# Performance work log

Measured on AMD Instinct MI355X. Metric: run time of the kernel, lower is better.

## Reference

```python
import jax, jax.numpy as jnp
import numpy as np

INPUT_DIM = 256
OUTPUT_DIM = 256
DEGREE = 7


def setup_inputs() -> dict:
    key = jax.random.key(0)
    k1, k2 = jax.random.split(key)
    x = jax.random.normal(k1, (16, 2048, INPUT_DIM), dtype=jnp.float32)
    std = 1.0 / (INPUT_DIM * (DEGREE + 1))
    hermite_coeffs = std * jax.random.normal(k2, (INPUT_DIM, OUTPUT_DIM, DEGREE + 1), dtype=jnp.float32)
    return {"x": x, "hermite_coeffs": hermite_coeffs}


def reference(x, hermite_coeffs):
    a, b, c = x.shape
    degree = hermite_coeffs.shape[2] - 1
    xf = jnp.tanh(x.reshape(-1, c))  # [N, input_dim]
    hs = [jnp.ones_like(xf)]
    if degree > 0:
        hs.append(2.0 * xf)
    for i in range(2, degree + 1):
        hs.append(2.0 * xf * hs[-1] - 2.0 * (i - 1) * hs[-2])
    hermite = jnp.stack(hs, axis=-1)  # [N, input_dim, degree+1]
    y = jnp.einsum('bid,iod->bo', hermite, hermite_coeffs)
    return y.reshape(a, b, hermite_coeffs.shape[1])
```

## Files before the change

kernel.cpp:

```cpp
#include <hip/hip_runtime.h>
#include <hip/hip_bf16.h>
#include <math.h>

#define INPUT_DIM 256
#define OUT_DIM   256
#define NDEG      8
#define KTOT      (INPUT_DIM * NDEG)
#define NROWS     (16 * 2048)

#define BM  128
#define BK  64
#define NK  (KTOT / BK)
#define SUPER 4
#define NSUP  (NK / SUPER)
#define CHUNK_ELEMS 16384

typedef __bf16 bf16x8 __attribute__((ext_vector_type(8)));
typedef float  f32x16 __attribute__((ext_vector_type(16)));

__global__ __launch_bounds__(256) void reorder_coeffs(const float* __restrict__ C,
                                                      __bf16* __restrict__ Bt) {
    int g = blockIdx.x * 256 + threadIdx.x;
    int i = g >> 8;
    int o = g & 255;
    const float4* src = (const float4*)(C + (size_t)i * (OUT_DIM * NDEG) + o * NDEG);
    float4 a = src[0];
    float4 b = src[1];
    bf16x8 v;
    v[0] = (__bf16)a.x; v[1] = (__bf16)a.y; v[2] = (__bf16)a.z; v[3] = (__bf16)a.w;
    v[4] = (__bf16)b.x; v[5] = (__bf16)b.y; v[6] = (__bf16)b.z; v[7] = (__bf16)b.w;
    int kc = i >> 3;
    int p  = i & 7;
    int s  = p >> 1;
    int hh = p & 1;
    int cc = o >> 6;
    int ni = (o >> 5) & 1;
    int l31 = o & 31;
    size_t dst = (size_t)kc * CHUNK_ELEMS + (s * 4 + cc) * 1024 + ni * 512 + hh * 256 + l31 * 8;
    *(bf16x8*)(Bt + dst) = v;
}

__device__ __forceinline__ bf16x8 featurize(float xs) {
    float e = __expf(2.0f * xs);
    float t = 1.0f - 2.0f / (e + 1.0f);
    bf16x8 v;
    float hm2 = 1.0f;
    float hm1 = 2.0f * t;
    v[0] = (__bf16)hm2;
    v[1] = (__bf16)hm1;
    #pragma unroll
    for (int d = 2; d < 8; ++d) {
        float h = 2.0f * t * hm1 - 2.0f * (float)(d - 1) * hm2;
        v[d] = (__bf16)h;
        hm2 = hm1; hm1 = h;
    }
    return v;
}

#define BARRIER() do {                                             \
    asm volatile("s_waitcnt lgkmcnt(0)" ::: "memory");             \
    __builtin_amdgcn_s_barrier();                                  \
    asm volatile("" ::: "memory");                                 \
} while (0)

__global__ __launch_bounds__(512, 2) void hermite_mfma(const float* __restrict__ x,
                                                       const __bf16* __restrict__ Bt,
                                                       float* __restrict__ out) {
    __shared__ __align__(16) __bf16 Alds[2][SUPER * 8192];

    const int tid  = threadIdx.x;
    const int bm   = blockIdx.x;
    const int wave = tid >> 6;
    const int mr   = wave >> 2;
    const int c    = wave & 3;
    const int lane = tid & 63;
    const int l31  = lane & 31;
    const int h    = lane >> 5;

    const int m  = tid & 127;
    const int pg = tid >> 7;
    const float* xptr = x + (size_t)(bm * BM + m) * INPUT_DIM + pg * 8;

    const __bf16* bbase = Bt + (size_t)c * 1024 + lane * 8;

    f32x16 acc[2][2] = {};
    bf16x8 bfr0[4][2];
    bf16x8 bfr1[4][2];

#define BLOAD(DST, KC)                                                       \
    if ((KC) < NK) {                                                         \
        const __bf16* g = bbase + (size_t)(KC) * CHUNK_ELEMS;                \
        _Pragma("unroll")                                                    \
        for (int s = 0; s < 4; ++s) {                                        \
            DST[s][0] = *(const bf16x8*)(g + s * 4096);                      \
            DST[s][1] = *(const bf16x8*)(g + s * 4096 + 512);                \
        }                                                                    \
    }

#define FEATW(NB, J, XS)                                                     \
    *(bf16x8*)(&Alds[NB][pg * 8192 + (J) * 1024 + m * 8]) = featurize(XS)

#define CHUNK_COMPUTE(CB, CC, CUR)                                           \
    _Pragma("unroll")                                                        \
    for (int s4 = 0; s4 < 4; ++s4) {                                         \
        bf16x8 af0 = *(const bf16x8*)(&Alds[CB][(CC) * 8192 + (2 * s4 + h) * 1024 + mr * 512 + l31 * 8]);       \
        bf16x8 af1 = *(const bf16x8*)(&Alds[CB][(CC) * 8192 + (2 * s4 + h) * 1024 + mr * 512 + 256 + l31 * 8]); \
        acc[0][0] = __builtin_amdgcn_mfma_f32_32x32x16_bf16(af0, CUR[s4][0], acc[0][0], 0, 0, 0); \
        acc[0][1] = __builtin_amdgcn_mfma_f32_32x32x16_bf16(af0, CUR[s4][1], acc[0][1], 0, 0, 0); \
        acc[1][0] = __builtin_amdgcn_mfma_f32_32x32x16_bf16(af1, CUR[s4][0], acc[1][0], 0, 0, 0); \
        acc[1][1] = __builtin_amdgcn_mfma_f32_32x32x16_bf16(af1, CUR[s4][1], acc[1][1], 0, 0, 0); \
    }

    float4 xq0 = *(const float4*)(xptr);
    float4 xq1 = *(const float4*)(xptr + 4);
    BLOAD(bfr0, 0);
    float4 xa0 = *(const float4*)(xptr + 32);
    float4 xa1 = *(const float4*)(xptr + 36);
    float4 xb0 = xa0, xb1 = xa1;
    FEATW(0, 0, xq0.x); FEATW(0, 1, xq0.y); FEATW(0, 2, xq0.z); FEATW(0, 3, xq0.w);
    FEATW(0, 4, xq1.x); FEATW(0, 5, xq1.y); FEATW(0, 6, xq1.z); FEATW(0, 7, xq1.w);
    BARRIER();

#define SUPER_STEP(S, CB, NB, XC0, XC1, XN0, XN1)                            \
    {                                                                        \
        const bool dofeat = (S) + 1 < NSUP;                                  \
        BLOAD(bfr1, (S) * 4 + 1);                                            \
        if (dofeat) { FEATW(NB, 0, XC0.x); FEATW(NB, 1, XC0.y); }            \
        CHUNK_COMPUTE(CB, 0, bfr0);                                          \
        BLOAD(bfr0, (S) * 4 + 2);                                            \
        if (dofeat) { FEATW(NB, 2, XC0.z); FEATW(NB, 3, XC0.w); }            \
        CHUNK_COMPUTE(CB, 1, bfr1);                                          \
        BLOAD(bfr1, (S) * 4 + 3);                                            \
        if (dofeat) { FEATW(NB, 4, XC1.x); FEATW(NB, 5, XC1.y); }            \
        CHUNK_COMPUTE(CB, 2, bfr0);                                          \
        BLOAD(bfr0, (S) * 4 + 4);                                            \
        if (dofeat) { FEATW(NB, 6, XC1.z); FEATW(NB, 7, XC1.w); }            \
        if ((S) + 2 < NSUP) {                                                \
            XN0 = *(const float4*)(xptr + ((S) + 2) * 32);                   \
            XN1 = *(const float4*)(xptr + ((S) + 2) * 32 + 4);               \
        }                                                                    \
        CHUNK_COMPUTE(CB, 3, bfr1);                                          \
        BARRIER();                                                           \
    }

    for (int sp = 0; sp < NSUP; sp += 2) {
        SUPER_STEP(sp,     0, 1, xa0, xa1, xb0, xb1);
        SUPER_STEP(sp + 1, 1, 0, xb0, xb1, xa0, xa1);
    }
#undef SUPER_STEP
#undef CHUNK_COMPUTE
#undef FEATW
#undef BLOAD

    #pragma unroll
    for (int mi = 0; mi < 2; ++mi)
        #pragma unroll
        for (int ni = 0; ni < 2; ++ni) {
            #pragma unroll
            for (int r = 0; r < 16; ++r) {
                int rl  = (r & 3) + 8 * (r >> 2) + 4 * h;
                int row = bm * BM + mr * 64 + mi * 32 + rl;
                out[(size_t)row * OUT_DIM + c * 64 + ni * 32 + l31] = acc[mi][ni][r];
            }
        }
}

extern "C" void kernel_launch(void* const* d_in, const int* in_sizes, int n_in,
                              void* d_out, int out_size, void* d_ws, size_t ws_size,
                              hipStream_t stream) {
    const float* x = (const float*)d_in[0];
    const float* C = (const float*)d_in[1];
    float* out = (float*)d_out;
    __bf16* Bt = (__bf16*)d_ws;

    reorder_coeffs<<<dim3((INPUT_DIM * OUT_DIM) / 256), dim3(256), 0, stream>>>(C, Bt);
    hermite_mfma<<<dim3(NROWS / BM), dim3(512), 0, stream>>>(x, Bt, out);
}
```

Measured before the change: 115.1 us.

## Halve row tile to 64 and raise occupancy to four blocks per CU

Cuts the M tile from 128 to 64 rows, so each wave computes one 32-row MFMA strip instead of two and each thread featurizes 4 inputs per super-step instead of 8. The LDS footprint halves and launch bounds ask for 4 blocks per CU, doubling the grid to 512 blocks. The goal is more waves and blocks in flight to hide latency and balance work across CUs. The cost is that each B fragment loaded from global memory feeds half as many MFMAs, which doubles total coefficient traffic.

```diff
diff --git a/kernel.cpp b/kernel.cpp
--- a/kernel.cpp
+++ b/kernel.cpp
@@ -8,12 +8,14 @@
 #define KTOT      (INPUT_DIM * NDEG)
 #define NROWS     (16 * 2048)
 
-#define BM  128
+#define BM  64
 #define BK  64
 #define NK  (KTOT / BK)
 #define SUPER 4
 #define NSUP  (NK / SUPER)
 #define CHUNK_ELEMS 16384
+#define APAGE 512
+#define ACHUNK (8 * APAGE)
 
 typedef __bf16 bf16x8 __attribute__((ext_vector_type(8)));
 typedef float  f32x16 __attribute__((ext_vector_type(16)));
@@ -35,7 +37,8 @@
     int hh = p & 1;
     int cc = o >> 6;
     int ni = (o >> 5) & 1;
-    int l31 = o & 31;
+    int l31 = o & 255 & 31;
+    l31 = o & 31;
     size_t dst = (size_t)kc * CHUNK_ELEMS + (s * 4 + cc) * 1024 + ni * 512 + hh * 256 + l31 * 8;
     *(bf16x8*)(Bt + dst) = v;
 }
@@ -63,10 +66,10 @@
     asm volatile("" ::: "memory");                                 \
 } while (0)
 
-__global__ __launch_bounds__(512, 2) void hermite_mfma(const float* __restrict__ x,
+__global__ __launch_bounds__(512, 4) void hermite_mfma(const float* __restrict__ x,
                                                        const __bf16* __restrict__ Bt,
                                                        float* __restrict__ out) {
-    __shared__ __align__(16) __bf16 Alds[2][SUPER * 8192];
+    __shared__ __align__(16) __bf16 Alds[2][SUPER * ACHUNK];
 
     const int tid  = threadIdx.x;
     const int bm   = blockIdx.x;
@@ -77,13 +80,13 @@
     const int l31  = lane & 31;
     const int h    = lane >> 5;
 
-    const int m  = tid & 127;
-    const int pg = tid >> 7;
-    const float* xptr = x + (size_t)(bm * BM + m) * INPUT_DIM + pg * 8;
+    const int m  = tid & 63;
+    const int pg = tid >> 6;
+    const float* xptr = x + (size_t)(bm * BM + m) * INPUT_DIM + pg * 4;
 
     const __bf16* bbase = Bt + (size_t)c * 1024 + lane * 8;
 
-    f32x16 acc[2][2] = {};
+    f32x16 acc[2] = {};
     bf16x8 bfr0[4][2];
     bf16x8 bfr1[4][2];
 
@@ -98,54 +101,47 @@
     }
 
 #define FEATW(NB, J, XS)                                                     \
-    *(bf16x8*)(&Alds[NB][pg * 8192 + (J) * 1024 + m * 8]) = featurize(XS)
+    *(bf16x8*)(&Alds[NB][(pg * 4 + (J)) * APAGE + m * 8]) = featurize(XS)
 
 #define CHUNK_COMPUTE(CB, CC, CUR)                                           \
     _Pragma("unroll")                                                        \
     for (int s4 = 0; s4 < 4; ++s4) {                                         \
-        bf16x8 af0 = *(const bf16x8*)(&Alds[CB][(CC) * 8192 + (2 * s4 + h) * 1024 + mr * 512 + l31 * 8]);       \
-        bf16x8 af1 = *(const bf16x8*)(&Alds[CB][(CC) * 8192 + (2 * s4 + h) * 1024 + mr * 512 + 256 + l31 * 8]); \
-        acc[0][0] = __builtin_amdgcn_mfma_f32_32x32x16_bf16(af0, CUR[s4][0], acc[0][0], 0, 0, 0); \
-        acc[0][1] = __builtin_amdgcn_mfma_f32_32x32x16_bf16(af0, CUR[s4][1], acc[0][1], 0, 0, 0); \
-        acc[1][0] = __builtin_amdgcn_mfma_f32_32x32x16_bf16(af1, CUR[s4][0], acc[1][0], 0, 0, 0); \
-        acc[1][1] = __builtin_amdgcn_mfma_f32_32x32x16_bf16(af1, CUR[s4][1], acc[1][1], 0, 0, 0); \
+        bf16x8 af = *(const bf16x8*)(&Alds[CB][((CC) * 8 + 2 * s4 + h) * APAGE + mr * 256 + l31 * 8]); \
+        acc[0] = __builtin_amdgcn_mfma_f32_32x32x16_bf16(af, CUR[s4][0], acc[0], 0, 0, 0); \
+        acc[1] = __builtin_amdgcn_mfma_f32_32x32x16_bf16(af, CUR[s4][1], acc[1], 0, 0, 0); \
     }
 
-    float4 xq0 = *(const float4*)(xptr);
-    float4 xq1 = *(const float4*)(xptr + 4);
+    float4 xq = *(const float4*)(xptr);
     BLOAD(bfr0, 0);
-    float4 xa0 = *(const float4*)(xptr + 32);
-    float4 xa1 = *(const float4*)(xptr + 36);
-    float4 xb0 = xa0, xb1 = xa1;
-    FEATW(0, 0, xq0.x); FEATW(0, 1, xq0.y); FEATW(0, 2, xq0.z); FEATW(0, 3, xq0.w);
-    FEATW(0, 4, xq1.x); FEATW(0, 5, xq1.y); FEATW(0, 6, xq1.z); FEATW(0, 7, xq1.w);
+    float4 xa = *(const float4*)(xptr + 32);
+    float4 xb = xa;
+    FEATW(0, 0, xq.x); FEATW(0, 1, xq.y); FEATW(0, 2, xq.z); FEATW(0, 3, xq.w);
     BARRIER();
 
-#define SUPER_STEP(S, CB, NB, XC0, XC1, XN0, XN1)                            \
+#define SUPER_STEP(S, CB, NB, XC, XN)                                        \
     {                                                                        \
         const bool dofeat = (S) + 1 < NSUP;                                  \
         BLOAD(bfr1, (S) * 4 + 1);                                            \
-        if (dofeat) { FEATW(NB, 0, XC0.x); FEATW(NB, 1, XC0.y); }            \
+        if (dofeat) { FEATW(NB, 0, XC.x); }                                  \
         CHUNK_COMPUTE(CB, 0, bfr0);                                          \
         BLOAD(bfr0, (S) * 4 + 2);                                            \
-        if (dofeat) { FEATW(NB, 2, XC0.z); FEATW(NB, 3, XC0.w); }            \
+        if (dofeat) { FEATW(NB, 1, XC.y); }                                  \
         CHUNK_COMPUTE(CB, 1, bfr1);                                          \
         BLOAD(bfr1, (S) * 4 + 3);                                            \
-        if (dofeat) { FEATW(NB, 4, XC1.x); FEATW(NB, 5, XC1.y); }            \
+        if (dofeat) { FEATW(NB, 2, XC.z); }                                  \
         CHUNK_COMPUTE(CB, 2, bfr0);                                          \
         BLOAD(bfr0, (S) * 4 + 4);                                            \
-        if (dofeat) { FEATW(NB, 6, XC1.z); FEATW(NB, 7, XC1.w); }            \
+        if (dofeat) { FEATW(NB, 3, XC.w); }                                  \
         if ((S) + 2 < NSUP) {                                                \
-            XN0 = *(const float4*)(xptr + ((S) + 2) * 32);                   \
-            XN1 = *(const float4*)(xptr + ((S) + 2) * 32 + 4);               \
+            XN = *(const float4*)(xptr + ((S) + 2) * 32);                    \
         }                                                                    \
         CHUNK_COMPUTE(CB, 3, bfr1);                                          \
         BARRIER();                                                           \
     }
 
     for (int sp = 0; sp < NSUP; sp += 2) {
-        SUPER_STEP(sp,     0, 1, xa0, xa1, xb0, xb1);
-        SUPER_STEP(sp + 1, 1, 0, xb0, xb1, xa0, xa1);
+        SUPER_STEP(sp,     0, 1, xa, xb);
+        SUPER_STEP(sp + 1, 1, 0, xb, xa);
     }
 #undef SUPER_STEP
 #undef CHUNK_COMPUTE
@@ -153,16 +149,14 @@
 #undef BLOAD
 
     #pragma unroll
-    for (int mi = 0; mi < 2; ++mi)
+    for (int ni = 0; ni < 2; ++ni) {
         #pragma unroll
-        for (int ni = 0; ni < 2; ++ni) {
-            #pragma unroll
-            for (int r = 0; r < 16; ++r) {
-                int rl  = (r & 3) + 8 * (r >> 2) + 4 * h;
-                int row = bm * BM + mr * 64 + mi * 32 + rl;
-                out[(size_t)row * OUT_DIM + c * 64 + ni * 32 + l31] = acc[mi][ni][r];
-            }
+        for (int r = 0; r < 16; ++r) {
+            int rl  = (r & 3) + 8 * (r >> 2) + 4 * h;
+            int row = bm * BM + mr * 32 + rl;
+            out[(size_t)row * OUT_DIM + c * 64 + ni * 32 + l31] = acc[ni][r];
         }
+    }
 }
 
 extern "C" void kernel_launch(void* const* d_in, const int* in_sizes, int n_in,
```

New measurement: 136.1 us. +18.2%, slower.

## Stagger featurization across even/odd waves and raise priority around MFMA blocks

Applied to the files above, without the earlier changes.

Even waves now featurize the next LDS buffer at the start of each super-step and odd waves do it after the second chunk, so the two wave groups sharing a SIMD alternate between VALU/transcendental work and MFMA work. Each MFMA chunk is also wrapped in s_setprio(1)/s_setprio(0) so waves issuing matrix ops are favoured by the scheduler. The intent is better overlap of the Hermite feature computation with matrix-core execution. The cost is two code paths, which grows code size and may raise register pressure, and the priority changes could delay the loads that feed later chunks.

```diff
diff --git a/kernel.cpp b/kernel.cpp
--- a/kernel.cpp
+++ b/kernel.cpp
@@ -101,14 +101,18 @@
     *(bf16x8*)(&Alds[NB][pg * 8192 + (J) * 1024 + m * 8]) = featurize(XS)
 
 #define CHUNK_COMPUTE(CB, CC, CUR)                                           \
-    _Pragma("unroll")                                                        \
-    for (int s4 = 0; s4 < 4; ++s4) {                                         \
-        bf16x8 af0 = *(const bf16x8*)(&Alds[CB][(CC) * 8192 + (2 * s4 + h) * 1024 + mr * 512 + l31 * 8]);       \
-        bf16x8 af1 = *(const bf16x8*)(&Alds[CB][(CC) * 8192 + (2 * s4 + h) * 1024 + mr * 512 + 256 + l31 * 8]); \
-        acc[0][0] = __builtin_amdgcn_mfma_f32_32x32x16_bf16(af0, CUR[s4][0], acc[0][0], 0, 0, 0); \
-        acc[0][1] = __builtin_amdgcn_mfma_f32_32x32x16_bf16(af0, CUR[s4][1], acc[0][1], 0, 0, 0); \
-        acc[1][0] = __builtin_amdgcn_mfma_f32_32x32x16_bf16(af1, CUR[s4][0], acc[1][0], 0, 0, 0); \
-        acc[1][1] = __builtin_amdgcn_mfma_f32_32x32x16_bf16(af1, CUR[s4][1], acc[1][1], 0, 0, 0); \
+    {                                                                        \
+        __builtin_amdgcn_s_setprio(1);                                       \
+        _Pragma("unroll")                                                    \
+        for (int s4 = 0; s4 < 4; ++s4) {                                     \
+            bf16x8 af0 = *(const bf16x8*)(&Alds[CB][(CC) * 8192 + (2 * s4 + h) * 1024 + mr * 512 + l31 * 8]);       \
+            bf16x8 af1 = *(const bf16x8*)(&Alds[CB][(CC) * 8192 + (2 * s4 + h) * 1024 + mr * 512 + 256 + l31 * 8]); \
+            acc[0][0] = __builtin_amdgcn_mfma_f32_32x32x16_bf16(af0, CUR[s4][0], acc[0][0], 0, 0, 0); \
+            acc[0][1] = __builtin_amdgcn_mfma_f32_32x32x16_bf16(af0, CUR[s4][1], acc[0][1], 0, 0, 0); \
+            acc[1][0] = __builtin_amdgcn_mfma_f32_32x32x16_bf16(af1, CUR[s4][0], acc[1][0], 0, 0, 0); \
+            acc[1][1] = __builtin_amdgcn_mfma_f32_32x32x16_bf16(af1, CUR[s4][1], acc[1][1], 0, 0, 0); \
+        }                                                                    \
+        __builtin_amdgcn_s_setprio(0);                                       \
     }
 
     float4 xq0 = *(const float4*)(xptr);
@@ -121,33 +125,63 @@
     FEATW(0, 4, xq1.x); FEATW(0, 5, xq1.y); FEATW(0, 6, xq1.z); FEATW(0, 7, xq1.w);
     BARRIER();
 
-#define SUPER_STEP(S, CB, NB, XC0, XC1, XN0, XN1)                            \
+#define SUPER_STEP_E(S, CB, NB, XC0, XC1, XN0, XN1)                          \
+    {                                                                        \
+        const bool dofeat = (S) + 1 < NSUP;                                  \
+        if (dofeat) { FEATW(NB, 0, XC0.x); FEATW(NB, 1, XC0.y);              \
+                      FEATW(NB, 2, XC0.z); FEATW(NB, 3, XC0.w); }            \
+        BLOAD(bfr1, (S) * 4 + 1);                                            \
+        if (dofeat) { FEATW(NB, 4, XC1.x); FEATW(NB, 5, XC1.y);              \
+                      FEATW(NB, 6, XC1.z); FEATW(NB, 7, XC1.w); }            \
+        CHUNK_COMPUTE(CB, 0, bfr0);                                          \
+        BLOAD(bfr0, (S) * 4 + 2);                                            \
+        CHUNK_COMPUTE(CB, 1, bfr1);                                          \
+        BLOAD(bfr1, (S) * 4 + 3);                                            \
+        CHUNK_COMPUTE(CB, 2, bfr0);                                          \
+        BLOAD(bfr0, (S) * 4 + 4);                                            \
+        if ((S) + 2 < NSUP) {                                                \
+            XN0 = *(const float4*)(xptr + ((S) + 2) * 32);                   \
+            XN1 = *(const float4*)(xptr + ((S) + 2) * 32 + 4);               \
+        }                                                                    \
+        CHUNK_COMPUTE(CB, 3, bfr1);                                          \
+        BARRIER();                                                           \
+    }
+
+#define SUPER_STEP_O(S, CB, NB, XC0, XC1, XN0, XN1)                          \
     {                                                                        \
         const bool dofeat = (S) + 1 < NSUP;                                  \
         BLOAD(bfr1, (S) * 4 + 1);                                            \
-        if (dofeat) { FEATW(NB, 0, XC0.x); FEATW(NB, 1, XC0.y); }            \
         CHUNK_COMPUTE(CB, 0, bfr0);                                          \
         BLOAD(bfr0, (S) * 4 + 2);                                            \
-        if (dofeat) { FEATW(NB, 2, XC0.z); FEATW(NB, 3, XC0.w); }            \
         CHUNK_COMPUTE(CB, 1, bfr1);                                          \
+        if (dofeat) { FEATW(NB, 0, XC0.x); FEATW(NB, 1, XC0.y);              \
+                      FEATW(NB, 2, XC0.z); FEATW(NB, 3, XC0.w);              \
+                      FEATW(NB, 4, XC1.x); FEATW(NB, 5, XC1.y);              \
+                      FEATW(NB, 6, XC1.z); FEATW(NB, 7, XC1.w); }            \
         BLOAD(bfr1, (S) * 4 + 3);                                            \
-        if (dofeat) { FEATW(NB, 4, XC1.x); FEATW(NB, 5, XC1.y); }            \
         CHUNK_COMPUTE(CB, 2, bfr0);                                          \
-        BLOAD(bfr0, (S) * 4 + 4);                                            \
-        if (dofeat) { FEATW(NB, 6, XC1.z); FEATW(NB, 7, XC1.w); }            \
         if ((S) + 2 < NSUP) {                                                \
             XN0 = *(const float4*)(xptr + ((S) + 2) * 32);                   \
             XN1 = *(const float4*)(xptr + ((S) + 2) * 32 + 4);               \
         }                                                                    \
+        BLOAD(bfr0, (S) * 4 + 4);                                            \
         CHUNK_COMPUTE(CB, 3, bfr1);                                          \
         BARRIER();                                                           \
     }
 
-    for (int sp = 0; sp < NSUP; sp += 2) {
-        SUPER_STEP(sp,     0, 1, xa0, xa1, xb0, xb1);
-        SUPER_STEP(sp + 1, 1, 0, xb0, xb1, xa0, xa1);
-    }
-#undef SUPER_STEP
+    if ((wave & 1) == 0) {
+        for (int sp = 0; sp < NSUP; sp += 2) {
+            SUPER_STEP_E(sp,     0, 1, xa0, xa1, xb0, xb1);
+            SUPER_STEP_E(sp + 1, 1, 0, xb0, xb1, xa0, xa1);
+        }
+    } else {
+        for (int sp = 0; sp < NSUP; sp += 2) {
+            SUPER_STEP_O(sp,     0, 1, xa0, xa1, xb0, xb1);
+            SUPER_STEP_O(sp + 1, 1, 0, xb0, xb1, xa0, xa1);
+        }
+    }
+#undef SUPER_STEP_E
+#undef SUPER_STEP_O
 #undef CHUNK_COMPUTE
 #undef FEATW
 #undef BLOAD
```

After: 117.0 us. About the same (+1.7%).

## Restructure K-loop into barrier-separated phases with batched LDS reads and MFMA priority

Applied to the files above, without the earlier changes.

Each chunk becomes a phase: all eight A fragments are read from LDS up front, then featurization writes and the next B global load are issued, then a workgroup barrier, then 16 MFMAs run at raised wave priority (s_setprio), then another waitcnt plus barrier. sched_barrier fences keep the compiler from interleaving memory and MFMA sections. The aim is to have waves alternate between memory and math phases so that MFMA issue is less often stalled by interleaved LDS and global traffic. The cost is two barriers per chunk instead of one per superstep, which adds synchronization overhead and more live registers.

```diff
diff --git a/kernel.cpp b/kernel.cpp
--- a/kernel.cpp
+++ b/kernel.cpp
@@ -57,12 +57,6 @@
     return v;
 }
 
-#define BARRIER() do {                                             \
-    asm volatile("s_waitcnt lgkmcnt(0)" ::: "memory");             \
-    __builtin_amdgcn_s_barrier();                                  \
-    asm volatile("" ::: "memory");                                 \
-} while (0)
-
 __global__ __launch_bounds__(512, 2) void hermite_mfma(const float* __restrict__ x,
                                                        const __bf16* __restrict__ Bt,
                                                        float* __restrict__ out) {
@@ -100,15 +94,52 @@
 #define FEATW(NB, J, XS)                                                     \
     *(bf16x8*)(&Alds[NB][pg * 8192 + (J) * 1024 + m * 8]) = featurize(XS)
 
-#define CHUNK_COMPUTE(CB, CC, CUR)                                           \
-    _Pragma("unroll")                                                        \
-    for (int s4 = 0; s4 < 4; ++s4) {                                         \
-        bf16x8 af0 = *(const bf16x8*)(&Alds[CB][(CC) * 8192 + (2 * s4 + h) * 1024 + mr * 512 + l31 * 8]);       \
-        bf16x8 af1 = *(const bf16x8*)(&Alds[CB][(CC) * 8192 + (2 * s4 + h) * 1024 + mr * 512 + 256 + l31 * 8]); \
-        acc[0][0] = __builtin_amdgcn_mfma_f32_32x32x16_bf16(af0, CUR[s4][0], acc[0][0], 0, 0, 0); \
-        acc[0][1] = __builtin_amdgcn_mfma_f32_32x32x16_bf16(af0, CUR[s4][1], acc[0][1], 0, 0, 0); \
-        acc[1][0] = __builtin_amdgcn_mfma_f32_32x32x16_bf16(af1, CUR[s4][0], acc[1][0], 0, 0, 0); \
-        acc[1][1] = __builtin_amdgcn_mfma_f32_32x32x16_bf16(af1, CUR[s4][1], acc[1][1], 0, 0, 0); \
+#define MFMA_S(AF0, AF1, CURS)                                               \
+    acc[0][0] = __builtin_amdgcn_mfma_f32_32x32x16_bf16(AF0, CURS[0], acc[0][0], 0, 0, 0); \
+    acc[0][1] = __builtin_amdgcn_mfma_f32_32x32x16_bf16(AF0, CURS[1], acc[0][1], 0, 0, 0); \
+    acc[1][0] = __builtin_amdgcn_mfma_f32_32x32x16_bf16(AF1, CURS[0], acc[1][0], 0, 0, 0); \
+    acc[1][1] = __builtin_amdgcn_mfma_f32_32x32x16_bf16(AF1, CURS[1], acc[1][1], 0, 0, 0);
+
+#define PHASE(S, CB, NB, CC, CUR, NXT, DOF, FJ, XS0, XS1, XPRE)              \
+    {                                                                        \
+        const __bf16* ab = &Alds[CB][(CC) * 8192 + mr * 512 + l31 * 8];      \
+        bf16x8 a0 = *(const bf16x8*)(ab + (0 + h) * 1024);                   \
+        bf16x8 a1 = *(const bf16x8*)(ab + (0 + h) * 1024 + 256);             \
+        bf16x8 a2 = *(const bf16x8*)(ab + (2 + h) * 1024);                   \
+        bf16x8 a3 = *(const bf16x8*)(ab + (2 + h) * 1024 + 256);             \
+        bf16x8 a4 = *(const bf16x8*)(ab + (4 + h) * 1024);                   \
+        bf16x8 a5 = *(const bf16x8*)(ab + (4 + h) * 1024 + 256);             \
+        bf16x8 a6 = *(const bf16x8*)(ab + (6 + h) * 1024);                   \
+        bf16x8 a7 = *(const bf16x8*)(ab + (6 + h) * 1024 + 256);             \
+        if (DOF) { FEATW(NB, (FJ), XS0); FEATW(NB, (FJ) + 1, XS1); }         \
+        BLOAD(NXT, (S) * 4 + (CC) + 1);                                      \
+        XPRE                                                                 \
+        __builtin_amdgcn_sched_barrier(0);                                   \
+        __builtin_amdgcn_s_barrier();                                        \
+        __builtin_amdgcn_sched_barrier(0);                                   \
+        __builtin_amdgcn_s_setprio(1);                                       \
+        MFMA_S(a0, a1, CUR[0])                                               \
+        MFMA_S(a2, a3, CUR[1])                                               \
+        MFMA_S(a4, a5, CUR[2])                                               \
+        MFMA_S(a6, a7, CUR[3])                                               \
+        __builtin_amdgcn_s_setprio(0);                                       \
+        __builtin_amdgcn_sched_barrier(0);                                   \
+        asm volatile("s_waitcnt lgkmcnt(0)" ::: "memory");                   \
+        __builtin_amdgcn_s_barrier();                                        \
+        asm volatile("" ::: "memory");                                       \
+    }
+
+#define SUPER_STEP(S, CB, NB, XC0, XC1, XN0, XN1)                            \
+    {                                                                        \
+        const bool dofeat = (S) + 1 < NSUP;                                  \
+        PHASE(S, CB, NB, 0, bfr0, bfr1, dofeat, 0, XC0.x, XC0.y, )           \
+        PHASE(S, CB, NB, 1, bfr1, bfr0, dofeat, 2, XC0.z, XC0.w, )           \
+        PHASE(S, CB, NB, 2, bfr0, bfr1, dofeat, 4, XC1.x, XC1.y, )           \
+        PHASE(S, CB, NB, 3, bfr1, bfr0, dofeat, 6, XC1.z, XC1.w,             \
+              if ((S) + 2 < NSUP) {                                          \
+                  XN0 = *(const float4*)(xptr + ((S) + 2) * 32);             \
+                  XN1 = *(const float4*)(xptr + ((S) + 2) * 32 + 4);         \
+              })                                                             \
     }
 
     float4 xq0 = *(const float4*)(xptr);
@@ -119,36 +150,17 @@
     float4 xb0 = xa0, xb1 = xa1;
     FEATW(0, 0, xq0.x); FEATW(0, 1, xq0.y); FEATW(0, 2, xq0.z); FEATW(0, 3, xq0.w);
     FEATW(0, 4, xq1.x); FEATW(0, 5, xq1.y); FEATW(0, 6, xq1.z); FEATW(0, 7, xq1.w);
-    BARRIER();
-
-#define SUPER_STEP(S, CB, NB, XC0, XC1, XN0, XN1)                            \
-    {                                                                        \
-        const bool dofeat = (S) + 1 < NSUP;                                  \
-        BLOAD(bfr1, (S) * 4 + 1);                                            \
-        if (dofeat) { FEATW(NB, 0, XC0.x); FEATW(NB, 1, XC0.y); }            \
-        CHUNK_COMPUTE(CB, 0, bfr0);                                          \
-        BLOAD(bfr0, (S) * 4 + 2);                                            \
-        if (dofeat) { FEATW(NB, 2, XC0.z); FEATW(NB, 3, XC0.w); }            \
-        CHUNK_COMPUTE(CB, 1, bfr1);                                          \
-        BLOAD(bfr1, (S) * 4 + 3);                                            \
-        if (dofeat) { FEATW(NB, 4, XC1.x); FEATW(NB, 5, XC1.y); }            \
-        CHUNK_COMPUTE(CB, 2, bfr0);                                          \
-        BLOAD(bfr0, (S) * 4 + 4);                                            \
-        if (dofeat) { FEATW(NB, 6, XC1.z); FEATW(NB, 7, XC1.w); }            \
-        if ((S) + 2 < NSUP) {                                                \
-            XN0 = *(const float4*)(xptr + ((S) + 2) * 32);                   \
-            XN1 = *(const float4*)(xptr + ((S) + 2) * 32 + 4);               \
-        }                                                                    \
-        CHUNK_COMPUTE(CB, 3, bfr1);                                          \
-        BARRIER();                                                           \
-    }
+    asm volatile("s_waitcnt lgkmcnt(0)" ::: "memory");
+    __builtin_amdgcn_s_barrier();
+    asm volatile("" ::: "memory");
 
     for (int sp = 0; sp < NSUP; sp += 2) {
         SUPER_STEP(sp,     0, 1, xa0, xa1, xb0, xb1);
         SUPER_STEP(sp + 1, 1, 0, xb0, xb1, xa0, xa1);
     }
 #undef SUPER_STEP
-#undef CHUNK_COMPUTE
+#undef PHASE
+#undef MFMA_S
 #undef FEATW
 #undef BLOAD
 
```

Measured after the change: 121.9 us. +5.9%, slower.
